# Kernel optimization log

Measured on AMD Instinct MI355X. Metric: run time of the kernel, lower is better.

The kernel has to match this reference:

```python
import jax, jax.numpy as jnp
import numpy as np

IN_CH, OUT_CH, K, STRIDE = 128, 256, 3, 1

def setup_inputs() -> dict:
    key = jax.random.key(0)
    kx, kw = jax.random.split(key)
    x = jax.random.normal(kx, (32, IN_CH, 56, 56), dtype=jnp.float32)
    # xavier_uniform: bound = sqrt(6 / (fan_in + fan_out)), fans include receptive field
    fan_in = IN_CH * K * K
    fan_out = OUT_CH * K * K
    bound = float(np.sqrt(6.0 / (fan_in + fan_out)))
    weight = jax.random.uniform(kw, (OUT_CH, IN_CH, K, K), dtype=jnp.float32,
                                minval=-bound, maxval=bound)
    bias = jnp.zeros((OUT_CH,), dtype=jnp.float32)
    return {"x": x, "weight": weight, "bias": bias}

def reference(x, weight, bias):
    # VALID (no-padding) conv, stride STRIDE, NCHW layout, OIHW kernel
    out = jax.lax.conv_general_dilated(
        x, weight,
        window_strides=(STRIDE, STRIDE),
        padding="VALID",
        dimension_numbers=("NCHW", "OIHW", "NCHW"))
    return out + bias[None, :, None, None]
```

## Files before the change

kernel.cpp:

```cpp
#include <hip/hip_runtime.h>
#include <hip/hip_bf16.h>
#include <stdint.h>

#define NB    32
#define CIN   128
#define HIN   56
#define HW    (HIN*HIN)
#define OCH   256
#define OHW   54
#define SPB   (OHW*OHW)
#define KSZ   (CIN*9)
#define BM    256
#define BN    128
#define BK    32
#define NKS   (KSZ/BK)
#define TOTC  (NB*SPB)
#define NT    729
#define GRAN  1536

typedef __attribute__((ext_vector_type(8))) short bf16x8;
typedef __attribute__((ext_vector_type(4))) float f32x4;

typedef __attribute__((address_space(1))) const uint32_t g_u32;
typedef __attribute__((address_space(3))) uint32_t l_u32;
static __device__ __forceinline__ void gl_lds16(const void* g, void* l) {
    __builtin_amdgcn_global_load_lds((g_u32*)g, (l_u32*)l, 16, 0, 0);
}

__global__ void xpose_cast(const float* __restrict__ x, __hip_bfloat16* __restrict__ xt) {
    __shared__ float tile[32][33];
    const int hw0 = blockIdx.x * 32;
    const int c0  = blockIdx.y * 32;
    const int n   = blockIdx.z;
    const int tx = threadIdx.x, ty = threadIdx.y;
    const float* xp = x + ((size_t)n*CIN + c0)*HW + hw0;
    #pragma unroll
    for (int i = ty; i < 32; i += 8)
        tile[i][tx] = xp[(size_t)i*HW + tx];
    __syncthreads();
    const int t = ty*32 + tx;
    const int hwl = t >> 3, q = t & 7;
    ushort4 v;
    v.x = __bfloat16_as_ushort(__float2bfloat16(tile[q*4+0][hwl]));
    v.y = __bfloat16_as_ushort(__float2bfloat16(tile[q*4+1][hwl]));
    v.z = __bfloat16_as_ushort(__float2bfloat16(tile[q*4+2][hwl]));
    v.w = __bfloat16_as_ushort(__float2bfloat16(tile[q*4+3][hwl]));
    __hip_bfloat16* op = xt + ((size_t)n*HW + hw0 + hwl)*CIN + c0 + q*4;
    *(ushort4*)op = v;
}

__global__ void wcast(const float* __restrict__ w, __hip_bfloat16* __restrict__ wt) {
    int tid = blockIdx.x*256 + threadIdx.x;
    if (tid >= OCH*KSZ) return;
    int oc = tid / KSZ, r = tid % KSZ;
    int pos = r >> 7, ic = r & 127;
    wt[tid] = __float2bfloat16(w[((size_t)(oc*CIN + ic))*9 + pos]);
}

__global__ __launch_bounds__(256, 2)
void conv_mfma(const __hip_bfloat16* __restrict__ xt,
               const __hip_bfloat16* __restrict__ wt,
               const float* __restrict__ bias,
               float* __restrict__ out) {
    __shared__ uint4 smem[3*GRAN];

    const int t = threadIdx.x;
    const int orig = blockIdx.x;
    const int xcd = orig & 7;
    const int tile = (xcd < 1 ? xcd*92 : 92 + (xcd-1)*91) + (orig >> 3);

    const int lane = t & 63, wid = t >> 6;
    const int wm = wid >> 1, wn = wid & 1;
    const int lr = lane & 15, lq = lane >> 4;

    const __hip_bfloat16* asrc[4];
    #pragma unroll
    for (int i = 0; i < 4; ++i) {
        int q = i*256 + t;
        int row = q >> 2, j = q & 3;
        int ls = j ^ ((row >> 1) & 3);
        asrc[i] = wt + (size_t)row*KSZ + ls*8;
    }
    const __hip_bfloat16* bsrc[2];
    #pragma unroll
    for (int i = 0; i < 2; ++i) {
        int q = i*256 + t;
        int col = q >> 2, j = q & 3;
        int ls = j ^ ((col >> 1) & 3);
        int colg = tile*BN + col;
        int n = colg / SPB, rem = colg - n*SPB;
        int oh = rem / OHW, ow = rem - oh*OHW;
        bsrc[i] = xt + ((size_t)(n*HIN + oh)*HIN + ow)*CIN + ls*8;
    }

    auto issueT = [&](uint4* dst, int ks) {
        const int aoff = ks*BK;
        const int pos = ks >> 2;
        const int kh = pos / 3, kw = pos - kh*3;
        const int boff = (kh*HIN + kw)*CIN + (ks & 3)*32;
        #pragma unroll
        for (int i = 0; i < 4; ++i) gl_lds16(asrc[i] + aoff, dst + i*256 + t);
        #pragma unroll
        for (int i = 0; i < 2; ++i) gl_lds16(bsrc[i] + boff, dst + 1024 + i*256 + t);
    };

    int ao[8], bo[4];
    #pragma unroll
    for (int mi = 0; mi < 8; ++mi) {
        int ra = wm*128 + mi*16 + lr;
        ao[mi] = ra*4 + (lq ^ ((ra >> 1) & 3));
    }
    #pragma unroll
    for (int ni = 0; ni < 4; ++ni) {
        int cb = wn*64 + ni*16 + lr;
        bo[ni] = 1024 + cb*4 + (lq ^ ((cb >> 1) & 3));
    }

    f32x4 acc[8][4];
    #pragma unroll
    for (int i = 0; i < 8; ++i)
        #pragma unroll
        for (int j = 0; j < 4; ++j)
            acc[i][j] = (f32x4){0.f, 0.f, 0.f, 0.f};

    #define MFMA_BF16 __builtin_amdgcn_mfma_f32_16x16x32_bf16

    uint4 *pR = smem, *pN = smem + GRAN, *pS = smem + 2*GRAN;

    issueT(pR, 0); issueT(pN, 1);
    asm volatile("s_waitcnt vmcnt(6)" ::: "memory");
    __builtin_amdgcn_s_barrier();
    __builtin_amdgcn_sched_barrier(0);

    for (int ks = 0; ks < NKS; ++ks) {
        bf16x8 aa[4], ab[4], bb[4];
        #pragma unroll
        for (int mi = 0; mi < 4; ++mi) aa[mi] = *(bf16x8*)&pR[ao[mi]];
        #pragma unroll
        for (int ni = 0; ni < 4; ++ni) bb[ni] = *(bf16x8*)&pR[bo[ni]];
        if (ks + 2 < NKS) issueT(pS, ks + 2);
        #pragma unroll
        for (int mi = 0; mi < 4; ++mi) ab[mi] = *(bf16x8*)&pR[ao[4 + mi]];

        asm volatile("s_waitcnt lgkmcnt(4)" ::: "memory");
        __builtin_amdgcn_sched_barrier(0);
        __builtin_amdgcn_s_setprio(1);
        #pragma unroll
        for (int mi = 0; mi < 4; ++mi)
            #pragma unroll
            for (int ni = 0; ni < 4; ++ni)
                acc[mi][ni] = MFMA_BF16(aa[mi], bb[ni], acc[mi][ni], 0, 0, 0);
        __builtin_amdgcn_s_setprio(0);

        asm volatile("s_waitcnt lgkmcnt(0)" ::: "memory");
        __builtin_amdgcn_sched_barrier(0);
        __builtin_amdgcn_s_setprio(1);
        #pragma unroll
        for (int mi = 0; mi < 4; ++mi)
            #pragma unroll
            for (int ni = 0; ni < 4; ++ni)
                acc[4+mi][ni] = MFMA_BF16(ab[mi], bb[ni], acc[4+mi][ni], 0, 0, 0);
        __builtin_amdgcn_s_setprio(0);

        if (ks + 1 < NKS) {
            if (ks + 2 < NKS) asm volatile("s_waitcnt vmcnt(6)" ::: "memory");
            else              asm volatile("s_waitcnt vmcnt(0)" ::: "memory");
            __builtin_amdgcn_s_barrier();
            __builtin_amdgcn_sched_barrier(0);
        }
        uint4* tmp = pR; pR = pN; pN = pS; pS = tmp;
    }

    __syncthreads();

    float (*eps)[132] = (float (*)[132])smem;
    const int cl4 = (t & 31) * 4;
    const int rsub = t >> 5;
    const int colg = tile*BN + cl4;
    const int nn = colg / SPB;
    const int sp = colg - nn*SPB;
    #pragma unroll
    for (int h = 0; h < 4; ++h) {
        if (wm == (h >> 1)) {
            const int mib = (h & 1) * 4;
            #pragma unroll
            for (int ii = 0; ii < 4; ++ii) {
                int rl = ii*16 + lq*4;
                #pragma unroll
                for (int ni = 0; ni < 4; ++ni) {
                    int cl = wn*64 + ni*16 + lr;
                    #pragma unroll
                    for (int r = 0; r < 4; ++r)
                        eps[rl + r][cl] = acc[mib + ii][ni][r];
                }
            }
        }
        __syncthreads();
        {
            #pragma unroll
            for (int pass = 0; pass < 8; ++pass) {
                int rl = pass*8 + rsub;
                int rg = h*64 + rl;
                f32x4 v = *(f32x4*)&eps[rl][cl4];
                v = v + bias[rg];
                *(f32x4*)&out[((size_t)nn*OCH + rg)*SPB + sp] = v;
            }
        }
        __syncthreads();
    }
}

__global__ void conv_naive(const float* __restrict__ x, const float* __restrict__ w,
                           const float* __restrict__ bias, float* __restrict__ out) {
    size_t tid = (size_t)blockIdx.x*256 + threadIdx.x;
    const size_t total = (size_t)NB*OCH*SPB;
    if (tid >= total) return;
    int col = (int)(tid % SPB);
    int oc  = (int)((tid / SPB) % OCH);
    int n   = (int)(tid / ((size_t)SPB*OCH));
    int oh = col / OHW, ow = col % OHW;
    float s = bias[oc];
    for (int ic = 0; ic < CIN; ++ic)
        #pragma unroll
        for (int kh = 0; kh < 3; ++kh)
            #pragma unroll
            for (int kw = 0; kw < 3; ++kw)
                s += x[((size_t)(n*CIN+ic)*HIN + oh+kh)*HIN + ow+kw]
                   * w[((size_t)(oc*CIN+ic)*3 + kh)*3 + kw];
    out[tid] = s;
}

extern "C" void kernel_launch(void* const* d_in, const int* in_sizes, int n_in,
                              void* d_out, int out_size, void* d_ws, size_t ws_size,
                              hipStream_t stream) {
    const float* x    = (const float*)d_in[0];
    const float* w    = (const float*)d_in[1];
    const float* bias = (const float*)d_in[2];
    float* out = (float*)d_out;

    const size_t xt_bytes = (size_t)NB*HW*CIN*sizeof(__hip_bfloat16);
    const size_t wt_bytes = (size_t)OCH*KSZ*sizeof(__hip_bfloat16);

    if (ws_size >= xt_bytes + wt_bytes) {
        __hip_bfloat16* xt  = (__hip_bfloat16*)d_ws;
        __hip_bfloat16* wtp = (__hip_bfloat16*)((char*)d_ws + xt_bytes);
        hipLaunchKernelGGL(xpose_cast, dim3(HW/32, CIN/32, NB), dim3(32, 8), 0, stream, x, xt);
        hipLaunchKernelGGL(wcast, dim3((OCH*KSZ + 255)/256), dim3(256), 0, stream, w, wtp);
        hipLaunchKernelGGL(conv_mfma, dim3(NT), dim3(256), 0, stream, xt, wtp, bias, out);
    } else {
        size_t total = (size_t)NB*OCH*SPB;
        hipLaunchKernelGGL(conv_naive, dim3((unsigned)((total + 255)/256)), dim3(256), 0, stream,
                           x, w, bias, out);
    }
}
```

Measured before the change: 84.14 us.

## Software-pipeline LDS fragment reads one k-step ahead with ping-pong registers

Restructures the main K loop into a two-step unrolled loop with even/odd register sets, so LDS reads for the next k-step are issued while the MFMAs for the current step run. This is meant to hide LDS read latency behind matrix math instead of waiting on lgkmcnt before each MFMA block. In exchange it doubles fragment register usage, which may lower occupancy or cause spills. It also waits on vmcnt(0) at each barrier, which removes some of the global-load overlap the old vmcnt(6) wait allowed.

```diff
diff --git a/kernel.cpp b/kernel.cpp
--- a/kernel.cpp
+++ b/kernel.cpp
@@ -124,51 +124,60 @@
             acc[i][j] = (f32x4){0.f, 0.f, 0.f, 0.f};
 
     #define MFMA_BF16 __builtin_amdgcn_mfma_f32_16x16x32_bf16
-
-    uint4 *pR = smem, *pN = smem + GRAN, *pS = smem + 2*GRAN;
-
-    issueT(pR, 0); issueT(pN, 1);
+    #define RD_AABB(AA, BB, P) \
+        _Pragma("unroll") for (int mi = 0; mi < 4; ++mi) AA[mi] = *(bf16x8*)&(P)[ao[mi]]; \
+        _Pragma("unroll") for (int ni = 0; ni < 4; ++ni) BB[ni] = *(bf16x8*)&(P)[bo[ni]];
+    #define RD_AB(AB, P) \
+        _Pragma("unroll") for (int mi = 0; mi < 4; ++mi) AB[mi] = *(bf16x8*)&(P)[ao[4 + mi]];
+    #define MFMA16LO(AA, BB) \
+        _Pragma("unroll") for (int mi = 0; mi < 4; ++mi) \
+            _Pragma("unroll") for (int ni = 0; ni < 4; ++ni) \
+                acc[mi][ni] = MFMA_BF16(AA[mi], BB[ni], acc[mi][ni], 0, 0, 0);
+    #define MFMA16HI(AB, BB) \
+        _Pragma("unroll") for (int mi = 0; mi < 4; ++mi) \
+            _Pragma("unroll") for (int ni = 0; ni < 4; ++ni) \
+                acc[4+mi][ni] = MFMA_BF16(AB[mi], BB[ni], acc[4+mi][ni], 0, 0, 0);
+    #define SCHEDB __builtin_amdgcn_sched_barrier(0)
+
+    uint4 *bcur = smem, *bnext = smem + GRAN, *bthird = smem + 2*GRAN;
+    bf16x8 aaE[4], abE[4], bbE[4];
+    bf16x8 aaO[4], abO[4], bbO[4];
+
+    issueT(bcur, 0); issueT(bnext, 1);
     asm volatile("s_waitcnt vmcnt(6)" ::: "memory");
     __builtin_amdgcn_s_barrier();
-    __builtin_amdgcn_sched_barrier(0);
-
-    for (int ks = 0; ks < NKS; ++ks) {
-        bf16x8 aa[4], ab[4], bb[4];
-        #pragma unroll
-        for (int mi = 0; mi < 4; ++mi) aa[mi] = *(bf16x8*)&pR[ao[mi]];
-        #pragma unroll
-        for (int ni = 0; ni < 4; ++ni) bb[ni] = *(bf16x8*)&pR[bo[ni]];
-        if (ks + 2 < NKS) issueT(pS, ks + 2);
-        #pragma unroll
-        for (int mi = 0; mi < 4; ++mi) ab[mi] = *(bf16x8*)&pR[ao[4 + mi]];
-
-        asm volatile("s_waitcnt lgkmcnt(4)" ::: "memory");
-        __builtin_amdgcn_sched_barrier(0);
-        __builtin_amdgcn_s_setprio(1);
-        #pragma unroll
-        for (int mi = 0; mi < 4; ++mi)
-            #pragma unroll
-            for (int ni = 0; ni < 4; ++ni)
-                acc[mi][ni] = MFMA_BF16(aa[mi], bb[ni], acc[mi][ni], 0, 0, 0);
-        __builtin_amdgcn_s_setprio(0);
-
-        asm volatile("s_waitcnt lgkmcnt(0)" ::: "memory");
-        __builtin_amdgcn_sched_barrier(0);
-        __builtin_amdgcn_s_setprio(1);
-        #pragma unroll
-        for (int mi = 0; mi < 4; ++mi)
-            #pragma unroll
-            for (int ni = 0; ni < 4; ++ni)
-                acc[4+mi][ni] = MFMA_BF16(ab[mi], bb[ni], acc[4+mi][ni], 0, 0, 0);
-        __builtin_amdgcn_s_setprio(0);
-
-        if (ks + 1 < NKS) {
-            if (ks + 2 < NKS) asm volatile("s_waitcnt vmcnt(6)" ::: "memory");
-            else              asm volatile("s_waitcnt vmcnt(0)" ::: "memory");
-            __builtin_amdgcn_s_barrier();
-            __builtin_amdgcn_sched_barrier(0);
+    SCHEDB;
+    RD_AABB(aaE, bbE, bcur)
+    RD_AB(abE, bcur)
+
+    for (int ks = 0; ks < NKS; ks += 2) {
+        asm volatile("s_waitcnt vmcnt(0)" ::: "memory");
+        __builtin_amdgcn_s_barrier();
+        SCHEDB;
+        if (ks + 2 < NKS) issueT(bthird, ks + 2);
+        RD_AABB(aaO, bbO, bnext)
+        asm volatile("s_waitcnt lgkmcnt(8)" ::: "memory");
+        SCHEDB;
+        MFMA16LO(aaE, bbE)
+        RD_AB(abO, bnext)
+        MFMA16HI(abE, bbE)
+        { uint4* tmp = bcur; bcur = bnext; bnext = bthird; bthird = tmp; }
+
+        asm volatile("s_waitcnt vmcnt(0)" ::: "memory");
+        __builtin_amdgcn_s_barrier();
+        SCHEDB;
+        if (ks + 3 < NKS) issueT(bthird, ks + 3);
+        if (ks + 2 < NKS) {
+            RD_AABB(aaE, bbE, bnext)
+            asm volatile("s_waitcnt lgkmcnt(8)" ::: "memory");
+        } else {
+            asm volatile("s_waitcnt lgkmcnt(0)" ::: "memory");
         }
-        uint4* tmp = pR; pR = pN; pN = pS; pS = tmp;
+        SCHEDB;
+        MFMA16LO(aaO, bbO)
+        if (ks + 2 < NKS) { RD_AB(abE, bnext) }
+        MFMA16HI(abO, bbO)
+        { uint4* tmp = bcur; bcur = bnext; bnext = bthird; bthird = tmp; }
     }
 
     __syncthreads();
```

Result: slower. 96.31 us (+14.5%).

## Load weight fragments directly to registers and stage only input tiles through LDS

Applied to the files above, without the earlier changes.

Replaces the triple-buffered global_load_lds pipeline that put both weight and input tiles in LDS. Each wave now reads its weight (A) fragments straight from global memory into registers. Input (B) tiles are loaded into registers and written to a double-buffered LDS area, and the k-loop is unrolled by two with a __syncthreads per step. The aim is to cut LDS traffic and footprint, but it adds register pressure, since two 8-fragment A sets are held, and global weight reads are redundant across the two waves that share a wm row.

```diff
diff --git a/kernel.cpp b/kernel.cpp
--- a/kernel.cpp
+++ b/kernel.cpp
@@ -16,16 +16,9 @@
 #define NKS   (KSZ/BK)
 #define TOTC  (NB*SPB)
 #define NT    729
-#define GRAN  1536
 
 typedef __attribute__((ext_vector_type(8))) short bf16x8;
 typedef __attribute__((ext_vector_type(4))) float f32x4;
-
-typedef __attribute__((address_space(1))) const uint32_t g_u32;
-typedef __attribute__((address_space(3))) uint32_t l_u32;
-static __device__ __forceinline__ void gl_lds16(const void* g, void* l) {
-    __builtin_amdgcn_global_load_lds((g_u32*)g, (l_u32*)l, 16, 0, 0);
-}
 
 __global__ void xpose_cast(const float* __restrict__ x, __hip_bfloat16* __restrict__ xt) {
     __shared__ float tile[32][33];
@@ -62,7 +55,7 @@
                const __hip_bfloat16* __restrict__ wt,
                const float* __restrict__ bias,
                float* __restrict__ out) {
-    __shared__ uint4 smem[3*GRAN];
+    __shared__ uint4 smem[2112];
 
     const int t = threadIdx.x;
     const int orig = blockIdx.x;
@@ -73,47 +66,31 @@
     const int wm = wid >> 1, wn = wid & 1;
     const int lr = lane & 15, lq = lane >> 4;
 
-    const __hip_bfloat16* asrc[4];
-    #pragma unroll
-    for (int i = 0; i < 4; ++i) {
-        int q = i*256 + t;
-        int row = q >> 2, j = q & 3;
-        int ls = j ^ ((row >> 1) & 3);
-        asrc[i] = wt + (size_t)row*KSZ + ls*8;
-    }
-    const __hip_bfloat16* bsrc[2];
-    #pragma unroll
-    for (int i = 0; i < 2; ++i) {
-        int q = i*256 + t;
-        int col = q >> 2, j = q & 3;
-        int ls = j ^ ((col >> 1) & 3);
-        int colg = tile*BN + col;
-        int n = colg / SPB, rem = colg - n*SPB;
-        int oh = rem / OHW, ow = rem - oh*OHW;
-        bsrc[i] = xt + ((size_t)(n*HIN + oh)*HIN + ow)*CIN + ls*8;
-    }
-
-    auto issueT = [&](uint4* dst, int ks) {
-        const int aoff = ks*BK;
-        const int pos = ks >> 2;
-        const int kh = pos / 3, kw = pos - kh*3;
-        const int boff = (kh*HIN + kw)*CIN + (ks & 3)*32;
-        #pragma unroll
-        for (int i = 0; i < 4; ++i) gl_lds16(asrc[i] + aoff, dst + i*256 + t);
-        #pragma unroll
-        for (int i = 0; i < 2; ++i) gl_lds16(bsrc[i] + boff, dst + 1024 + i*256 + t);
-    };
-
-    int ao[8], bo[4];
-    #pragma unroll
-    for (int mi = 0; mi < 8; ++mi) {
-        int ra = wm*128 + mi*16 + lr;
-        ao[mi] = ra*4 + (lq ^ ((ra >> 1) & 3));
-    }
+    int aidx[8];
+    #pragma unroll
+    for (int mi = 0; mi < 8; ++mi)
+        aidx[mi] = (wm*128 + mi*16 + lr)*KSZ + lq*8;
+
+    const __hip_bfloat16* bsrc0;
+    const __hip_bfloat16* bsrc1;
+    {
+        int q0 = t, c0i = q0 >> 2, j0 = q0 & 3;
+        int l0 = j0 ^ ((c0i >> 1) & 3);
+        int cg0 = tile*BN + c0i;
+        int n0 = cg0 / SPB, r0 = cg0 - n0*SPB;
+        bsrc0 = xt + ((size_t)(n0*HIN + r0/OHW)*HIN + r0%OHW)*CIN + l0*8;
+        int q1 = 256 + t, c1i = q1 >> 2, j1 = q1 & 3;
+        int l1 = j1 ^ ((c1i >> 1) & 3);
+        int cg1 = tile*BN + c1i;
+        int n1 = cg1 / SPB, r1 = cg1 - n1*SPB;
+        bsrc1 = xt + ((size_t)(n1*HIN + r1/OHW)*HIN + r1%OHW)*CIN + l1*8;
+    }
+
+    int bo[4];
     #pragma unroll
     for (int ni = 0; ni < 4; ++ni) {
         int cb = wn*64 + ni*16 + lr;
-        bo[ni] = 1024 + cb*4 + (lq ^ ((cb >> 1) & 3));
+        bo[ni] = cb*4 + (lq ^ ((cb >> 1) & 3));
     }
 
     f32x4 acc[8][4];
@@ -124,54 +101,57 @@
             acc[i][j] = (f32x4){0.f, 0.f, 0.f, 0.f};
 
     #define MFMA_BF16 __builtin_amdgcn_mfma_f32_16x16x32_bf16
-
-    uint4 *pR = smem, *pN = smem + GRAN, *pS = smem + 2*GRAN;
-
-    issueT(pR, 0); issueT(pN, 1);
-    asm volatile("s_waitcnt vmcnt(6)" ::: "memory");
-    __builtin_amdgcn_s_barrier();
-    __builtin_amdgcn_sched_barrier(0);
-
-    for (int ks = 0; ks < NKS; ++ks) {
-        bf16x8 aa[4], ab[4], bb[4];
-        #pragma unroll
-        for (int mi = 0; mi < 4; ++mi) aa[mi] = *(bf16x8*)&pR[ao[mi]];
-        #pragma unroll
-        for (int ni = 0; ni < 4; ++ni) bb[ni] = *(bf16x8*)&pR[bo[ni]];
-        if (ks + 2 < NKS) issueT(pS, ks + 2);
-        #pragma unroll
-        for (int mi = 0; mi < 4; ++mi) ab[mi] = *(bf16x8*)&pR[ao[4 + mi]];
-
-        asm volatile("s_waitcnt lgkmcnt(4)" ::: "memory");
-        __builtin_amdgcn_sched_barrier(0);
-        __builtin_amdgcn_s_setprio(1);
-        #pragma unroll
-        for (int mi = 0; mi < 4; ++mi)
-            #pragma unroll
-            for (int ni = 0; ni < 4; ++ni)
-                acc[mi][ni] = MFMA_BF16(aa[mi], bb[ni], acc[mi][ni], 0, 0, 0);
+    #define BOFF(KS) (((KS) >> 2) / 3 * HIN + ((KS) >> 2) % 3) * CIN + ((KS) & 3)*32
+    #define LOADB(KS) do { \
+        const int _o = BOFF(KS); \
+        s0 = *(const uint4*)(bsrc0 + _o); \
+        s1 = *(const uint4*)(bsrc1 + _o); } while (0)
+    #define WRITEB(KS) do { \
+        uint4* _d = smem + ((KS) & 1)*512; \
+        _d[t] = s0; _d[256 + t] = s1; } while (0)
+    #define LDA(ARR, KS) \
+        _Pragma("unroll") for (int mi = 0; mi < 8; ++mi) \
+            ARR[mi] = *(const bf16x8*)(wt + aidx[mi] + (KS)*BK);
+    #define MFMA32(ACUR) \
+        __builtin_amdgcn_s_setprio(1); \
+        _Pragma("unroll") for (int mi = 0; mi < 8; ++mi) \
+            _Pragma("unroll") for (int ni = 0; ni < 4; ++ni) \
+                acc[mi][ni] = MFMA_BF16(ACUR[mi], bb[ni], acc[mi][ni], 0, 0, 0); \
         __builtin_amdgcn_s_setprio(0);
 
-        asm volatile("s_waitcnt lgkmcnt(0)" ::: "memory");
-        __builtin_amdgcn_sched_barrier(0);
-        __builtin_amdgcn_s_setprio(1);
-        #pragma unroll
-        for (int mi = 0; mi < 4; ++mi)
-            #pragma unroll
-            for (int ni = 0; ni < 4; ++ni)
-                acc[4+mi][ni] = MFMA_BF16(ab[mi], bb[ni], acc[4+mi][ni], 0, 0, 0);
-        __builtin_amdgcn_s_setprio(0);
-
-        if (ks + 1 < NKS) {
-            if (ks + 2 < NKS) asm volatile("s_waitcnt vmcnt(6)" ::: "memory");
-            else              asm volatile("s_waitcnt vmcnt(0)" ::: "memory");
-            __builtin_amdgcn_s_barrier();
-            __builtin_amdgcn_sched_barrier(0);
-        }
-        uint4* tmp = pR; pR = pN; pN = pS; pS = tmp;
-    }
-
+    bf16x8 aE[8], aO[8];
+    uint4 s0, s1;
+
+    LOADB(0);
+    WRITEB(0);
+    LOADB(1);
+    LDA(aE, 0)
     __syncthreads();
+
+    for (int ks = 0; ks < NKS; ks += 2) {
+        {
+            WRITEB(ks + 1);
+            if (ks + 2 < NKS) LOADB(ks + 2);
+            LDA(aO, ks + 1)
+            bf16x8 bb[4];
+            const uint4* bp = smem + 0;
+            #pragma unroll
+            for (int ni = 0; ni < 4; ++ni) bb[ni] = *(const bf16x8*)&bp[bo[ni]];
+            MFMA32(aE)
+            __syncthreads();
+        }
+        {
+            if (ks + 2 < NKS) WRITEB(ks + 2);
+            if (ks + 3 < NKS) LOADB(ks + 3);
+            if (ks + 2 < NKS) { LDA(aE, ks + 2) }
+            bf16x8 bb[4];
+            const uint4* bp = smem + 512;
+            #pragma unroll
+            for (int ni = 0; ni < 4; ++ni) bb[ni] = *(const bf16x8*)&bp[bo[ni]];
+            MFMA32(aO)
+            __syncthreads();
+        }
+    }
 
     float (*eps)[132] = (float (*)[132])smem;
     const int cl4 = (t & 31) * 4;
```

Measured after the change: 139.7 us. 66.0% more time.

## Switch conv GEMM to 32x32x16 MFMA and merge prep kernels

Applied to the files above, without the earlier changes.

Replaces the 16x16x32 bf16 MFMA tiling with 32x32x16 MFMA. Each BK=32 step is split into two K halves read from swizzled LDS, and the epilogue register-to-row mapping is rewritten to match. Separately, the transpose-cast and weight-cast kernels are merged into one launch to save launch overhead. The larger MFMA cuts LDS read traffic and instruction count per FLOP, at the risk of LDS bank conflicts in the new access pattern and different scheduling.

```diff
diff --git a/kernel.cpp b/kernel.cpp
--- a/kernel.cpp
+++ b/kernel.cpp
@@ -18,8 +18,12 @@
 #define NT    729
 #define GRAN  1536
 
+#define XPB   (98*4*NB)
+#define WCB   ((OCH*KSZ)/256)
+
 typedef __attribute__((ext_vector_type(8))) short bf16x8;
 typedef __attribute__((ext_vector_type(4))) float f32x4;
+typedef __attribute__((ext_vector_type(16))) float f32x16;
 
 typedef __attribute__((address_space(1))) const uint32_t g_u32;
 typedef __attribute__((address_space(3))) uint32_t l_u32;
@@ -27,34 +31,36 @@
     __builtin_amdgcn_global_load_lds((g_u32*)g, (l_u32*)l, 16, 0, 0);
 }
 
-__global__ void xpose_cast(const float* __restrict__ x, __hip_bfloat16* __restrict__ xt) {
+__global__ void prep(const float* __restrict__ x, __hip_bfloat16* __restrict__ xt,
+                     const float* __restrict__ w, __hip_bfloat16* __restrict__ wt) {
     __shared__ float tile[32][33];
-    const int hw0 = blockIdx.x * 32;
-    const int c0  = blockIdx.y * 32;
-    const int n   = blockIdx.z;
-    const int tx = threadIdx.x, ty = threadIdx.y;
-    const float* xp = x + ((size_t)n*CIN + c0)*HW + hw0;
-    #pragma unroll
-    for (int i = ty; i < 32; i += 8)
-        tile[i][tx] = xp[(size_t)i*HW + tx];
-    __syncthreads();
-    const int t = ty*32 + tx;
-    const int hwl = t >> 3, q = t & 7;
-    ushort4 v;
-    v.x = __bfloat16_as_ushort(__float2bfloat16(tile[q*4+0][hwl]));
-    v.y = __bfloat16_as_ushort(__float2bfloat16(tile[q*4+1][hwl]));
-    v.z = __bfloat16_as_ushort(__float2bfloat16(tile[q*4+2][hwl]));
-    v.w = __bfloat16_as_ushort(__float2bfloat16(tile[q*4+3][hwl]));
-    __hip_bfloat16* op = xt + ((size_t)n*HW + hw0 + hwl)*CIN + c0 + q*4;
-    *(ushort4*)op = v;
-}
-
-__global__ void wcast(const float* __restrict__ w, __hip_bfloat16* __restrict__ wt) {
-    int tid = blockIdx.x*256 + threadIdx.x;
-    if (tid >= OCH*KSZ) return;
-    int oc = tid / KSZ, r = tid % KSZ;
-    int pos = r >> 7, ic = r & 127;
-    wt[tid] = __float2bfloat16(w[((size_t)(oc*CIN + ic))*9 + pos]);
+    const int bid = blockIdx.x;
+    const int t = threadIdx.x;
+    if (bid < XPB) {
+        const int hwb = bid % 98;
+        const int cb  = (bid / 98) & 3;
+        const int n   = bid / 392;
+        const int hw0 = hwb * 32, c0 = cb * 32;
+        const int tx = t & 31, ty = t >> 5;
+        const float* xp = x + ((size_t)n*CIN + c0)*HW + hw0;
+        #pragma unroll
+        for (int i = ty; i < 32; i += 8)
+            tile[i][tx] = xp[(size_t)i*HW + tx];
+        __syncthreads();
+        const int hwl = t >> 3, q = t & 7;
+        ushort4 v;
+        v.x = __bfloat16_as_ushort(__float2bfloat16(tile[q*4+0][hwl]));
+        v.y = __bfloat16_as_ushort(__float2bfloat16(tile[q*4+1][hwl]));
+        v.z = __bfloat16_as_ushort(__float2bfloat16(tile[q*4+2][hwl]));
+        v.w = __bfloat16_as_ushort(__float2bfloat16(tile[q*4+3][hwl]));
+        __hip_bfloat16* op = xt + ((size_t)n*HW + hw0 + hwl)*CIN + c0 + q*4;
+        *(ushort4*)op = v;
+    } else {
+        int tid = (bid - XPB)*256 + t;
+        int oc = tid / KSZ, r = tid % KSZ;
+        int pos = r >> 7, ic = r & 127;
+        wt[tid] = __float2bfloat16(w[((size_t)(oc*CIN + ic))*9 + pos]);
+    }
 }
 
 __global__ __launch_bounds__(256, 2)
@@ -71,7 +77,8 @@
 
     const int lane = t & 63, wid = t >> 6;
     const int wm = wid >> 1, wn = wid & 1;
-    const int lr = lane & 15, lq = lane >> 4;
+    const int r32 = lane & 31, khalf = lane >> 5;
+    const int lq = lane >> 4;
 
     const __hip_bfloat16* asrc[4];
     #pragma unroll
@@ -104,26 +111,26 @@
         for (int i = 0; i < 2; ++i) gl_lds16(bsrc[i] + boff, dst + 1024 + i*256 + t);
     };
 
-    int ao[8], bo[4];
-    #pragma unroll
-    for (int mi = 0; mi < 8; ++mi) {
-        int ra = wm*128 + mi*16 + lr;
-        ao[mi] = ra*4 + (lq ^ ((ra >> 1) & 3));
-    }
-    #pragma unroll
-    for (int ni = 0; ni < 4; ++ni) {
-        int cb = wn*64 + ni*16 + lr;
-        bo[ni] = 1024 + cb*4 + (lq ^ ((cb >> 1) & 3));
-    }
-
-    f32x4 acc[8][4];
-    #pragma unroll
-    for (int i = 0; i < 8; ++i)
-        #pragma unroll
-        for (int j = 0; j < 4; ++j)
-            acc[i][j] = (f32x4){0.f, 0.f, 0.f, 0.f};
-
-    #define MFMA_BF16 __builtin_amdgcn_mfma_f32_16x16x32_bf16
+    int ao[4], bo[2];
+    #pragma unroll
+    for (int mi = 0; mi < 4; ++mi) {
+        int ra = wm*128 + mi*32 + r32;
+        ao[mi] = ra*4 + (khalf ^ ((ra >> 1) & 3));
+    }
+    #pragma unroll
+    for (int ni = 0; ni < 2; ++ni) {
+        int cb = wn*64 + ni*32 + r32;
+        bo[ni] = 1024 + cb*4 + (khalf ^ ((cb >> 1) & 3));
+    }
+
+    f32x16 acc[4][2];
+    #pragma unroll
+    for (int i = 0; i < 4; ++i)
+        #pragma unroll
+        for (int j = 0; j < 2; ++j)
+            acc[i][j] = (f32x16)(0.f);
+
+    #define MFMA32x32 __builtin_amdgcn_mfma_f32_32x32x16_bf16
 
     uint4 *pR = smem, *pN = smem + GRAN, *pS = smem + 2*GRAN;
 
@@ -133,23 +140,25 @@
     __builtin_amdgcn_sched_barrier(0);
 
     for (int ks = 0; ks < NKS; ++ks) {
-        bf16x8 aa[4], ab[4], bb[4];
-        #pragma unroll
-        for (int mi = 0; mi < 4; ++mi) aa[mi] = *(bf16x8*)&pR[ao[mi]];
-        #pragma unroll
-        for (int ni = 0; ni < 4; ++ni) bb[ni] = *(bf16x8*)&pR[bo[ni]];
+        bf16x8 a0[4], a1[4], b0[2], b1[2];
+        #pragma unroll
+        for (int mi = 0; mi < 4; ++mi) a0[mi] = *(bf16x8*)&pR[ao[mi]];
+        #pragma unroll
+        for (int ni = 0; ni < 2; ++ni) b0[ni] = *(bf16x8*)&pR[bo[ni]];
         if (ks + 2 < NKS) issueT(pS, ks + 2);
         #pragma unroll
-        for (int mi = 0; mi < 4; ++mi) ab[mi] = *(bf16x8*)&pR[ao[4 + mi]];
-
-        asm volatile("s_waitcnt lgkmcnt(4)" ::: "memory");
+        for (int mi = 0; mi < 4; ++mi) a1[mi] = *(bf16x8*)&pR[ao[mi] ^ 2];
+        #pragma unroll
+        for (int ni = 0; ni < 2; ++ni) b1[ni] = *(bf16x8*)&pR[bo[ni] ^ 2];
+
+        asm volatile("s_waitcnt lgkmcnt(6)" ::: "memory");
         __builtin_amdgcn_sched_barrier(0);
         __builtin_amdgcn_s_setprio(1);
         #pragma unroll
         for (int mi = 0; mi < 4; ++mi)
             #pragma unroll
-            for (int ni = 0; ni < 4; ++ni)
-                acc[mi][ni] = MFMA_BF16(aa[mi], bb[ni], acc[mi][ni], 0, 0, 0);
+            for (int ni = 0; ni < 2; ++ni)
+                acc[mi][ni] = MFMA32x32(a0[mi], b0[ni], acc[mi][ni], 0, 0, 0);
         __builtin_amdgcn_s_setprio(0);
 
         asm volatile("s_waitcnt lgkmcnt(0)" ::: "memory");
@@ -158,8 +167,8 @@
         #pragma unroll
         for (int mi = 0; mi < 4; ++mi)
             #pragma unroll
-            for (int ni = 0; ni < 4; ++ni)
-                acc[4+mi][ni] = MFMA_BF16(ab[mi], bb[ni], acc[4+mi][ni], 0, 0, 0);
+            for (int ni = 0; ni < 2; ++ni)
+                acc[mi][ni] = MFMA32x32(a1[mi], b1[ni], acc[mi][ni], 0, 0, 0);
         __builtin_amdgcn_s_setprio(0);
 
         if (ks + 1 < NKS) {
@@ -179,19 +188,22 @@
     const int colg = tile*BN + cl4;
     const int nn = colg / SPB;
     const int sp = colg - nn*SPB;
+    (void)lq;
     #pragma unroll
     for (int h = 0; h < 4; ++h) {
         if (wm == (h >> 1)) {
-            const int mib = (h & 1) * 4;
-            #pragma unroll
-            for (int ii = 0; ii < 4; ++ii) {
-                int rl = ii*16 + lq*4;
+            const int hs = h & 1;
+            #pragma unroll
+            for (int mp = 0; mp < 2; ++mp) {
+                const int mi = hs*2 + mp;
                 #pragma unroll
-                for (int ni = 0; ni < 4; ++ni) {
-                    int cl = wn*64 + ni*16 + lr;
+                for (int ni = 0; ni < 2; ++ni) {
+                    const int cl = wn*64 + ni*32 + r32;
                     #pragma unroll
-                    for (int r = 0; r < 4; ++r)
-                        eps[rl + r][cl] = acc[mib + ii][ni][r];
+                    for (int reg = 0; reg < 16; ++reg) {
+                        int crow = (reg & 3) + 8*(reg >> 2) + 4*khalf;
+                        eps[mp*32 + crow][cl] = acc[mi][ni][reg];
+                    }
                 }
             }
         }
@@ -244,8 +256,7 @@
     if (ws_size >= xt_bytes + wt_bytes) {
         __hip_bfloat16* xt  = (__hip_bfloat16*)d_ws;
         __hip_bfloat16* wtp = (__hip_bfloat16*)((char*)d_ws + xt_bytes);
-        hipLaunchKernelGGL(xpose_cast, dim3(HW/32, CIN/32, NB), dim3(32, 8), 0, stream, x, xt);
-        hipLaunchKernelGGL(wcast, dim3((OCH*KSZ + 255)/256), dim3(256), 0, stream, w, wtp);
+        hipLaunchKernelGGL(prep, dim3(XPB + WCB), dim3(256), 0, stream, x, xt, w, wtp);
         hipLaunchKernelGGL(conv_mfma, dim3(NT), dim3(256), 0, stream, xt, wtp, bias, out);
     } else {
         size_t total = (size_t)NB*OCH*SPB;
```

New measurement: 89.63 us. 1.07x slower.
